# Optimization experiments

Hardware: AMD Instinct MI355X
Metric: run time of the kernel (lower is better)

The kernel has to match this reference:

```python
import jax, jax.numpy as jnp
import numpy as np

NEG_SLOPE = 0.2


def _seg_sum(x, ids, n):
    return jax.ops.segment_sum(x, ids, num_segments=n)


def _seg_softmax(score, ids, n):
    # numerically stable segment softmax over segments `ids`
    m = jax.ops.segment_max(score, ids, num_segments=n)
    ex = jnp.exp(score - m[ids])
    denom = _seg_sum(ex, ids, n)
    return ex / denom[ids]


def _seg_mean(x, ids, n):
    s = _seg_sum(x, ids, n)
    cnt = _seg_sum(jnp.ones(ids.shape[0], x.dtype), ids, n)
    return jnp.where(cnt[:, None] > 0, s / jnp.maximum(cnt, 1.0)[:, None], 0.0)


def _dphgnn(X, V, E, S, Wx, bx, Wv, bv, a, Wt, bt, num_nodes, num_edges):
    X_init = X @ Wx + bx                         # [N, H]
    X_feat = X @ Wv + bv                         # [N, H]
    score_node = X_feat @ a                      # [N]
    score = jax.nn.leaky_relu(score_node[V], NEG_SLOPE)   # [nnz]
    w = _seg_softmax(score, E, num_edges)        # [nnz]
    Xev = X_feat[V] * w[:, None]                 # [nnz, H] gather + weight
    Y_v2e = jax.nn.elu(_seg_sum(Xev, E, num_edges))       # [M, H]
    e_msg = jnp.concatenate([Y_v2e, S], axis=1)  # [M, H+star]
    Y = e_msg @ Wt + bt                          # [M, H]
    Xn = _seg_mean(Y[E], V, num_nodes)           # [N, H]
    Xn = jax.nn.elu(Xn)                          # is_last=False, dropout=eval
    return Xn + X_init


def _hyperconv(X, V, E, Wf, bf, num_nodes, num_edges):
    Xn = X @ Wf + bf
    Y = _seg_mean(Xn[V], E, num_edges)           # [M, O]
    ones = jnp.ones(V.shape[0], jnp.float32)
    D_v = _seg_sum(ones, V, num_nodes)           # node degrees
    cnt_e = _seg_sum(ones, E, num_edges)
    # torch scatter_reduce(mean, include_self=True): zero init counts as one element
    De = _seg_sum(D_v[V], E, num_edges) / (cnt_e + 1.0)
    De_inv = jnp.where(De > 0, De ** -0.5, 1.0)
    Y = De_inv[:, None] * Y
    Xo = _seg_sum(Y[E], V, num_nodes)
    Dv_inv = jnp.where(D_v > 0, D_v ** -0.5, 0.0)
    return Dv_inv[:, None] * Xo                  # is_last=True: no relu/dropout


def setup_inputs() -> dict:
    key = jax.random.key(0)
    ks = jax.random.split(key, 24)
    N, M, NNZ = 50000, 20000, 400000
    IN, H, OUT, STAR = 128, 256, 128, 64

    def lin(k, i, o):
        s = 1.0 / np.sqrt(i)
        k1, k2 = jax.random.split(k)
        return (jax.random.uniform(k1, (i, o), jnp.float32, -s, s),
                jax.random.uniform(k2, (o,), jnp.float32, -s, s))

    X = jax.random.normal(ks[0], (N, IN), jnp.float32)
    V = jax.random.randint(ks[1], (NNZ,), 0, N).at[-1].set(N - 1)
    E = jax.random.randint(ks[2], (NNZ,), 0, M).at[-1].set(M - 1)
    S = jax.random.normal(ks[3], (M, STAR), jnp.float32)

    Wx0, bx0 = lin(ks[4], IN, H)
    Wv0, bv0 = lin(ks[5], IN, H)
    a0 = jax.random.uniform(ks[6], (H,), jnp.float32, -1/np.sqrt(H), 1/np.sqrt(H))
    Wt0, bt0 = lin(ks[7], H + STAR, H)
    Wx1, bx1 = lin(ks[8], H, H)
    Wv1, bv1 = lin(ks[9], H, H)
    a1 = jax.random.uniform(ks[10], (H,), jnp.float32, -1/np.sqrt(H), 1/np.sqrt(H))
    Wt1, bt1 = lin(ks[11], H + STAR, H)
    Wf, bf = lin(ks[12], H, OUT)

    return dict(X=X, V=V, E=E, S=S,
                Wx0=Wx0, bx0=bx0, Wv0=Wv0, bv0=bv0, a0=a0, Wt0=Wt0, bt0=bt0,
                Wx1=Wx1, bx1=bx1, Wv1=Wv1, bv1=bv1, a1=a1, Wt1=Wt1, bt1=bt1,
                Wf=Wf, bf=bf)


def reference(X, V, E, S, Wx0, bx0, Wv0, bv0, a0, Wt0, bt0,
              Wx1, bx1, Wv1, bv1, a1, Wt1, bt1, Wf, bf):
    N = X.shape[0]
    M = S.shape[0]
    h = _dphgnn(X, V, E, S, Wx0, bx0, Wv0, bv0, a0, Wt0, bt0, N, M)
    h = _dphgnn(h, V, E, S, Wx1, bx1, Wv1, bv1, a1, Wt1, bt1, N, M)
    out = _hyperconv(h, V, E, Wf, bf, N, M)
    return out
```

## Files before the change

### kernel.cpp

```cpp
#include <hip/hip_runtime.h>

typedef unsigned short u16;
typedef __attribute__((ext_vector_type(4))) u16 u16x4;
typedef __attribute__((ext_vector_type(8))) u16 u16x8;
typedef __attribute__((ext_vector_type(8))) _Float16 f16x8;
typedef __attribute__((ext_vector_type(4))) float f32x4;

__device__ __forceinline__ u16 f2h(float x) {
    _Float16 h = (_Float16)x;
    return __builtin_bit_cast(u16, h);
}
__device__ __forceinline__ float h2f(u16 u) {
    return (float)__builtin_bit_cast(_Float16, u);
}

__device__ __forceinline__ void gl_lds16(const void* g, void* l) {
    __builtin_amdgcn_global_load_lds(
        (const __attribute__((address_space(1))) void*)g,
        (__attribute__((address_space(3))) void*)l, 16, 0, 0);
}

__global__ __launch_bounds__(256) void gemm_mfma_kernel(
    const u16* __restrict__ A, int lda,
    const u16* __restrict__ B, int ldb,
    const float* __restrict__ biasF, const float* __restrict__ biasB,
    u16* __restrict__ CbA, u16* __restrict__ CbB,
    const float* __restrict__ avec, float* __restrict__ scoreOut,
    const int* __restrict__ tKey, const int* __restrict__ tVal,
    int* __restrict__ tCur, int* __restrict__ tOut, int tNnz, int tailBlocks,
    int M, int Nc, int ncSplit, int K, int nrb, int ncb)
{
    if ((int)blockIdx.x < tailBlocks) {
        int k0 = ((int)blockIdx.x * 256 + (int)threadIdx.x) * 8;
        if (k0 >= tNnz) return;
        int kmax = min(tNnz - k0, 8);
        int kk[8], vv[8], sl[8];
        if (kmax == 8) {
            int4 a = *(const int4*)(tKey + k0), b = *(const int4*)(tKey + k0 + 4);
            int4 c = *(const int4*)(tVal + k0), d = *(const int4*)(tVal + k0 + 4);
            kk[0]=a.x; kk[1]=a.y; kk[2]=a.z; kk[3]=a.w; kk[4]=b.x; kk[5]=b.y; kk[6]=b.z; kk[7]=b.w;
            vv[0]=c.x; vv[1]=c.y; vv[2]=c.z; vv[3]=c.w; vv[4]=d.x; vv[5]=d.y; vv[6]=d.z; vv[7]=d.w;
        } else {
            for (int q = 0; q < kmax; ++q) { kk[q] = tKey[k0 + q]; vv[q] = tVal[k0 + q]; }
        }
        for (int q = 0; q < kmax; ++q) sl[q] = atomicAdd(&tCur[kk[q]], 1);
        for (int q = 0; q < kmax; ++q) tOut[sl[q]] = vv[q];
        return;
    }
    int g = (int)blockIdx.x - tailBlocks;
    int xcd = g & 7;
    int slot = g >> 3;
    int rbi = slot / ncb;
    int cb = slot - rbi * ncb;
    int rb = xcd + 8 * rbi;
    if (rb >= nrb) return;

    __shared__ __align__(16) u16 lds[12288];
    u16* sA0 = lds;
    u16* sA1 = lds + 4096;
    u16* sB0 = lds + 8192;
    u16* sB1 = lds + 10240;

    int tid = threadIdx.x;
    int wave = tid >> 6, lane = tid & 63;
    int row0 = rb * 128, col0 = cb * 64;

    long gA[2];
    int sOffA[2];
#pragma unroll
    for (int r = 0; r < 2; ++r) {
        int trow = r * 64 + wave * 16 + (lane >> 2);
        int chunk = (lane & 3) ^ ((trow >> 2) & 3);
        int arow = min(row0 + trow, M - 1);
        gA[r] = (long)arow * lda + chunk * 8;
        sOffA[r] = (r * 64 + wave * 16) * 32;
    }
    int trowB = wave * 16 + (lane >> 2);
    int chunkB = (lane & 3) ^ ((trowB >> 2) & 3);
    long gB = (long)(col0 + trowB) * ldb + chunkB * 8;
    int sOffB = (wave * 16) * 32;

    int m16 = lane & 15, quad = lane >> 4;
    int offA[4], offB[2];
#pragma unroll
    for (int i = 0; i < 4; ++i) {
        int ra = (wave & 1) * 64 + i * 16 + m16;
        offA[i] = ra * 32 + ((quad ^ ((ra >> 2) & 3)) * 8);
    }
#pragma unroll
    for (int j = 0; j < 2; ++j) {
        int rbx = (wave >> 1) * 32 + j * 16 + m16;
        offB[j] = rbx * 32 + ((quad ^ ((rbx >> 2) & 3)) * 8);
    }

    f32x4 acc[4][2];
#pragma unroll
    for (int i = 0; i < 4; ++i)
#pragma unroll
        for (int j = 0; j < 2; ++j) {
            f32x4 z = {0.f, 0.f, 0.f, 0.f};
            acc[i][j] = z;
        }

    int nkb = K >> 6;
    for (int kb = 0; kb < nkb; ++kb) {
#pragma unroll
        for (int r = 0; r < 2; ++r) {
            gl_lds16(A + gA[r], sA0 + sOffA[r]);
            gl_lds16(A + gA[r] + 32, sA1 + sOffA[r]);
        }
        gl_lds16(B + gB, sB0 + sOffB);
        gl_lds16(B + gB + 32, sB1 + sOffB);
        __syncthreads();
        {
            f16x8 av[4], bv[2];
#pragma unroll
            for (int i = 0; i < 4; ++i) av[i] = *(const f16x8*)(sA0 + offA[i]);
#pragma unroll
            for (int j = 0; j < 2; ++j) bv[j] = *(const f16x8*)(sB0 + offB[j]);
#pragma unroll
            for (int i = 0; i < 4; ++i)
#pragma unroll
                for (int j = 0; j < 2; ++j)
                    acc[i][j] = __builtin_amdgcn_mfma_f32_16x16x32_f16(av[i], bv[j], acc[i][j], 0, 0, 0);
        }
        {
            f16x8 av[4], bv[2];
#pragma unroll
            for (int i = 0; i < 4; ++i) av[i] = *(const f16x8*)(sA1 + offA[i]);
#pragma unroll
            for (int j = 0; j < 2; ++j) bv[j] = *(const f16x8*)(sB1 + offB[j]);
#pragma unroll
            for (int i = 0; i < 4; ++i)
#pragma unroll
                for (int j = 0; j < 2; ++j)
                    acc[i][j] = __builtin_amdgcn_mfma_f32_16x16x32_f16(av[i], bv[j], acc[i][j], 0, 0, 0);
        }
        __syncthreads();
#pragma unroll
        for (int r = 0; r < 2; ++r) gA[r] += 64;
        gB += 64;
    }

    int rbase = (wave & 1) * 64, cbase = (wave >> 1) * 32;
    float bj[2];
#pragma unroll
    for (int j = 0; j < 2; ++j) {
        int col = col0 + cbase + j * 16 + m16;
        bj[j] = (col >= ncSplit) ? biasB[col - ncSplit] : biasF[col];
    }
    u16* wlds = lds + wave * 2560;
    __syncthreads();
#pragma unroll
    for (int j = 0; j < 2; ++j)
#pragma unroll
        for (int i = 0; i < 4; ++i)
#pragma unroll
            for (int rr = 0; rr < 4; ++rr) {
                int lr = i * 16 + quad * 4 + rr;
                int lc = j * 16 + m16;
                int seg = (lc >> 3) ^ ((lr >> 2) & 3);
                wlds[lr * 40 + seg * 8 + (lc & 7)] = f2h(acc[i][j][rr] + bj[j]);
            }
    __syncthreads();
    {
        int colbase = col0 + cbase;
        bool isB = (colbase >= ncSplit);
        u16* Cp = isB ? CbB : CbA;
        int stride = isB ? (Nc - ncSplit) : ncSplit;
        int cc = isB ? (colbase - ncSplit) : colbase;
        bool doScore = (scoreOut != nullptr) && isB;
        int row = row0 + rbase + lane;
        if (row < M) {
            float sp = 0.f;
#pragma unroll
            for (int s = 0; s < 4; ++s) {
                int sseg = s ^ ((lane >> 2) & 3);
                u16x8 vv = *(const u16x8*)(wlds + lane * 40 + sseg * 8);
                *(u16x8*)(Cp + (size_t)row * stride + cc + s * 8) = vv;
                if (doScore) {
#pragma unroll
                    for (int q = 0; q < 8; ++q)
                        sp += h2f(vv[q]) * avec[cc + s * 8 + q];
                }
            }
            if (doScore) atomicAdd(scoreOut + row, sp);
        }
    }
}

struct WJob { const float* W; u16* Wt; int K; int ncShift; };
struct WJobs { WJob j[7]; };

__global__ void prep_fused_kernel(
    const int* __restrict__ V, const int* __restrict__ E,
    int* __restrict__ ecnt, int* __restrict__ ncnt, int nnz, int nbCnt,
    const float* __restrict__ X, u16* __restrict__ Abuf, int n4x,
    const float* __restrict__ S, u16* __restrict__ Ae, int nS, int nbCast,
    WJobs jobs)
{
    int b = blockIdx.x;
    if (b < nbCnt) {
        int k0 = (b * 256 + (int)threadIdx.x) * 8;
        if (k0 >= nnz) return;
        int kmax = min(nnz - k0, 8);
        int vv[8], ee[8];
        if (kmax == 8) {
            int4 a = *(const int4*)(V + k0), bb = *(const int4*)(V + k0 + 4);
            int4 c = *(const int4*)(E + k0), d = *(const int4*)(E + k0 + 4);
            vv[0]=a.x; vv[1]=a.y; vv[2]=a.z; vv[3]=a.w; vv[4]=bb.x; vv[5]=bb.y; vv[6]=bb.z; vv[7]=bb.w;
            ee[0]=c.x; ee[1]=c.y; ee[2]=c.z; ee[3]=c.w; ee[4]=d.x; ee[5]=d.y; ee[6]=d.z; ee[7]=d.w;
        } else {
            for (int q = 0; q < kmax; ++q) { vv[q] = V[k0 + q]; ee[q] = E[k0 + q]; }
        }
        for (int q = 0; q < kmax; ++q) atomicAdd(&ecnt[ee[q]], 1);
        for (int q = 0; q < kmax; ++q) atomicAdd(&ncnt[vv[q]], 1);
        return;
    }
    if (b < nbCnt + nbCast) {
        int id = (b - nbCnt) * 256 + (int)threadIdx.x;
        if (id < n4x) {
            float4 x = ((const float4*)X)[id];
            u16x4 h;
            h.x = f2h(x.x); h.y = f2h(x.y); h.z = f2h(x.z); h.w = f2h(x.w);
            *(u16x4*)(Abuf + (size_t)id * 4) = h;
        } else {
            int i = id - n4x;
            if (i < nS) {
                int e = i >> 6, c = i & 63;
                Ae[(size_t)e * 320 + 256 + c] = f2h(S[i]);
            }
        }
        return;
    }
    int bb = b - nbCnt - nbCast;
    int job = bb / 320, rem = bb - job * 320;
    WJob jb = jobs.j[job];
    int Nc = 1 << jb.ncShift;
    int idx = rem * 256 + (int)threadIdx.x;
    if (idx >= jb.K * Nc) return;
    int k = idx >> jb.ncShift, n = idx & (Nc - 1);
    jb.Wt[(size_t)n * jb.K + k] = f2h(jb.W[idx]);
}

__global__ __launch_bounds__(256) void scan_part1_dual(
    const int* __restrict__ cntE, int* __restrict__ offE, int* __restrict__ psumE, int nE, int nbE,
    const int* __restrict__ cntN, int* __restrict__ offN, int* __restrict__ psumN, int nN)
{
    const int* cnt; int* off; int* psum; int n; int b;
    if ((int)blockIdx.x < nbE) { cnt = cntE; off = offE; psum = psumE; n = nE; b = blockIdx.x; }
    else { cnt = cntN; off = offN; psum = psumN; n = nN; b = blockIdx.x - nbE; }

    __shared__ int tsum[256];
    int base = b * 1024;
    int t = threadIdx.x;
    int idx0 = base + t * 4;
    int4 c = make_int4(0, 0, 0, 0);
    if (idx0 + 3 < n) c = *(const int4*)(cnt + idx0);
    else {
        if (idx0 + 0 < n) c.x = cnt[idx0 + 0];
        if (idx0 + 1 < n) c.y = cnt[idx0 + 1];
        if (idx0 + 2 < n) c.z = cnt[idx0 + 2];
        if (idx0 + 3 < n) c.w = cnt[idx0 + 3];
    }
    int s = c.x + c.y + c.z + c.w;
    tsum[t] = s;
    __syncthreads();
    for (int o = 1; o < 256; o <<= 1) {
        int v = (t >= o) ? tsum[t - o] : 0;
        __syncthreads();
        tsum[t] += v;
        __syncthreads();
    }
    int run = tsum[t] - s;
    run += c.x; if (idx0 + 0 < n) off[idx0 + 1] = run;
    run += c.y; if (idx0 + 1 < n) off[idx0 + 2] = run;
    run += c.z; if (idx0 + 2 < n) off[idx0 + 3] = run;
    run += c.w; if (idx0 + 3 < n) off[idx0 + 4] = run;
    if (t == 255) psum[b] = tsum[255];
}

__global__ __launch_bounds__(256) void scan_part2_dual(
    const int* __restrict__ cntE, int* __restrict__ offE, const int* __restrict__ psumE,
    int* __restrict__ curE, int nE, int nbE,
    const int* __restrict__ cntN, int* __restrict__ offN, const int* __restrict__ psumN,
    int* __restrict__ curN, int nN)
{
    const int* cnt; int* off; const int* psum; int* cur; int n; int b;
    if ((int)blockIdx.x < nbE) { cnt = cntE; off = offE; psum = psumE; cur = curE; n = nE; b = blockIdx.x; }
    else { cnt = cntN; off = offN; psum = psumN; cur = curN; n = nN; b = blockIdx.x - nbE; }

    __shared__ int bpref;
    int t = threadIdx.x;
    if (t < 64) {
        int s = (t < b) ? psum[t] : 0;
#pragma unroll
        for (int o = 32; o; o >>= 1) s += __shfl_xor(s, o);
        if (t == 0) {
            bpref = s;
            if (b == 0) off[0] = 0;
        }
    }
    __syncthreads();
    int base = b * 1024 + t * 4;
#pragma unroll
    for (int q = 0; q < 4; ++q) {
        int i = base + q;
        if (i < n) {
            int inc = off[i + 1] + bpref;
            off[i + 1] = inc;
            cur[i] = inc - cnt[i];
        }
    }
}

__device__ __forceinline__ float lrelu(float s) { return s >= 0.f ? s : 0.2f * s; }

__global__ void v2e_fused_kernel(const u16* __restrict__ Xf,
                                 const float* __restrict__ score,
                                 const int* __restrict__ eoff,
                                 const int* __restrict__ edge_v,
                                 u16* __restrict__ Ae, int M)
{
    int e = blockIdx.x * 8 + (threadIdx.x >> 5);
    if (e >= M) return;
    int sl = threadIdx.x & 31;
    int j0 = eoff[e], j1 = eoff[e + 1];
    float m = -INFINITY;
    for (int j = j0 + sl; j < j1; j += 32) m = fmaxf(m, lrelu(score[edge_v[j]]));
#pragma unroll
    for (int o = 16; o; o >>= 1) m = fmaxf(m, __shfl_xor(m, o));
    float sum = 0.f;
    for (int j = j0 + sl; j < j1; j += 32) sum += expf(lrelu(score[edge_v[j]]) - m);
#pragma unroll
    for (int o = 16; o; o >>= 1) sum += __shfl_xor(sum, o);
    float inv = (j1 > j0) ? 1.0f / sum : 0.f;

    float acc[8] = {0.f, 0.f, 0.f, 0.f, 0.f, 0.f, 0.f, 0.f};
    int col = sl * 8;
    int j = j0;
    for (; j + 3 < j1; j += 4) {
        int v0 = edge_v[j + 0], v1 = edge_v[j + 1], v2 = edge_v[j + 2], v3 = edge_v[j + 3];
        float s0 = score[v0], s1 = score[v1], s2 = score[v2], s3 = score[v3];
        u16x8 r0 = *(const u16x8*)(Xf + (size_t)v0 * 256 + col);
        u16x8 r1 = *(const u16x8*)(Xf + (size_t)v1 * 256 + col);
        u16x8 r2 = *(const u16x8*)(Xf + (size_t)v2 * 256 + col);
        u16x8 r3 = *(const u16x8*)(Xf + (size_t)v3 * 256 + col);
        float w0 = expf(lrelu(s0) - m) * inv;
        float w1 = expf(lrelu(s1) - m) * inv;
        float w2 = expf(lrelu(s2) - m) * inv;
        float w3 = expf(lrelu(s3) - m) * inv;
#pragma unroll
        for (int q = 0; q < 8; ++q) {
            acc[q] += h2f(r0[q]) * w0;
            acc[q] += h2f(r1[q]) * w1;
            acc[q] += h2f(r2[q]) * w2;
            acc[q] += h2f(r3[q]) * w3;
        }
    }
    for (; j < j1; ++j) {
        int v = edge_v[j];
        float ww = expf(lrelu(score[v]) - m) * inv;
        u16x8 r = *(const u16x8*)(Xf + (size_t)v * 256 + col);
#pragma unroll
        for (int q = 0; q < 8; ++q) acc[q] += h2f(r[q]) * ww;
    }
    u16x8 hv;
#pragma unroll
    for (int q = 0; q < 8; ++q) {
        float vq = acc[q];
        vq = vq > 0.f ? vq : expm1f(vq);
        hv[q] = f2h(vq);
    }
    *(u16x8*)(Ae + (size_t)e * 320 + col) = hv;
}

__global__ void e2v_finish_kernel(const u16* __restrict__ Y,
                                  const int* __restrict__ noff,
                                  const int* __restrict__ node_e,
                                  const u16* __restrict__ Xinit,
                                  u16* __restrict__ H, int N,
                                  float* __restrict__ zbuf, int zN, int zTail)
{
    if ((int)blockIdx.x < zTail) {
        int id = (int)blockIdx.x * 256 + (int)threadIdx.x;
        if (id < zN) zbuf[id] = 0.f;
        return;
    }
    int v = ((int)blockIdx.x - zTail) * 8 + (threadIdx.x >> 5);
    if (v >= N) return;
    int sl = threadIdx.x & 31;
    int col = sl * 8;
    int i0 = noff[v], i1 = noff[v + 1];
    float acc[8] = {0.f, 0.f, 0.f, 0.f, 0.f, 0.f, 0.f, 0.f};
    int i = i0;
    for (; i + 3 < i1; i += 4) {
        int e0 = node_e[i + 0], e1 = node_e[i + 1], e2 = node_e[i + 2], e3 = node_e[i + 3];
        u16x8 r0 = *(const u16x8*)(Y + (size_t)e0 * 256 + col);
        u16x8 r1 = *(const u16x8*)(Y + (size_t)e1 * 256 + col);
        u16x8 r2 = *(const u16x8*)(Y + (size_t)e2 * 256 + col);
        u16x8 r3 = *(const u16x8*)(Y + (size_t)e3 * 256 + col);
#pragma unroll
        for (int q = 0; q < 8; ++q) {
            acc[q] += h2f(r0[q]);
            acc[q] += h2f(r1[q]);
            acc[q] += h2f(r2[q]);
            acc[q] += h2f(r3[q]);
        }
    }
    for (; i < i1; ++i) {
        int e = node_e[i];
        u16x8 r = *(const u16x8*)(Y + (size_t)e * 256 + col);
#pragma unroll
        for (int q = 0; q < 8; ++q) acc[q] += h2f(r[q]);
    }
    float inv = (i1 > i0) ? 1.0f / (float)(i1 - i0) : 0.f;
    size_t base = (size_t)v * 256 + col;
    u16x8 xi = *(const u16x8*)(Xinit + base);
    u16x8 hv;
#pragma unroll
    for (int q = 0; q < 8; ++q) {
        float mm = acc[q] * inv;
        float oq = (mm > 0.f ? mm : expm1f(mm)) + h2f(xi[q]);
        hv[q] = f2h(oq);
    }
    *(u16x8*)(H + base) = hv;
}

__global__ void yh_kernel(const u16* __restrict__ Xc,
                          const int* __restrict__ eoff, const int* __restrict__ edge_v,
                          const int* __restrict__ noff, u16* __restrict__ Yh, int M)
{
    int e = blockIdx.x * 16 + (threadIdx.x >> 4);
    if (e >= M) return;
    int sl = threadIdx.x & 15;
    int col = sl * 8;
    int j0 = eoff[e], j1 = eoff[e + 1];

    float dsum = 0.f;
    for (int j = j0 + sl; j < j1; j += 16) {
        int v = edge_v[j];
        dsum += (float)(noff[v + 1] - noff[v]);
    }
#pragma unroll
    for (int o = 8; o; o >>= 1) dsum += __shfl_xor(dsum, o);
    float De = dsum / ((float)(j1 - j0) + 1.0f);
    float deinv = De > 0.f ? rsqrtf(De) : 1.0f;

    float acc[8] = {0.f, 0.f, 0.f, 0.f, 0.f, 0.f, 0.f, 0.f};
    int j = j0;
    for (; j + 3 < j1; j += 4) {
        int v0 = edge_v[j + 0], v1 = edge_v[j + 1], v2 = edge_v[j + 2], v3 = edge_v[j + 3];
        u16x8 r0 = *(const u16x8*)(Xc + (size_t)v0 * 128 + col);
        u16x8 r1 = *(const u16x8*)(Xc + (size_t)v1 * 128 + col);
        u16x8 r2 = *(const u16x8*)(Xc + (size_t)v2 * 128 + col);
        u16x8 r3 = *(const u16x8*)(Xc + (size_t)v3 * 128 + col);
#pragma unroll
        for (int q = 0; q < 8; ++q) {
            acc[q] += h2f(r0[q]);
            acc[q] += h2f(r1[q]);
            acc[q] += h2f(r2[q]);
            acc[q] += h2f(r3[q]);
        }
    }
    for (; j < j1; ++j) {
        int v = edge_v[j];
        u16x8 r = *(const u16x8*)(Xc + (size_t)v * 128 + col);
#pragma unroll
        for (int q = 0; q < 8; ++q) acc[q] += h2f(r[q]);
    }
    float sc = ((j1 > j0) ? 1.0f / (float)(j1 - j0) : 0.f) * deinv;
    u16x8 o8;
#pragma unroll
    for (int q = 0; q < 8; ++q) o8[q] = f2h(acc[q] * sc);
    *(u16x8*)(Yh + (size_t)e * 128 + col) = o8;
}

__global__ void xo_final_kernel(const u16* __restrict__ Yh,
                                const int* __restrict__ noff, const int* __restrict__ node_e,
                                float* __restrict__ out, int N)
{
    int v = blockIdx.x * 16 + (threadIdx.x >> 4);
    if (v >= N) return;
    int sl = threadIdx.x & 15;
    int col = sl * 8;
    int i0 = noff[v], i1 = noff[v + 1];
    float acc[8] = {0.f, 0.f, 0.f, 0.f, 0.f, 0.f, 0.f, 0.f};
    int i = i0;
    for (; i + 3 < i1; i += 4) {
        int e0 = node_e[i + 0], e1 = node_e[i + 1], e2 = node_e[i + 2], e3 = node_e[i + 3];
        u16x8 r0 = *(const u16x8*)(Yh + (size_t)e0 * 128 + col);
        u16x8 r1 = *(const u16x8*)(Yh + (size_t)e1 * 128 + col);
        u16x8 r2 = *(const u16x8*)(Yh + (size_t)e2 * 128 + col);
        u16x8 r3 = *(const u16x8*)(Yh + (size_t)e3 * 128 + col);
#pragma unroll
        for (int q = 0; q < 8; ++q) {
            acc[q] += h2f(r0[q]);
            acc[q] += h2f(r1[q]);
            acc[q] += h2f(r2[q]);
            acc[q] += h2f(r3[q]);
        }
    }
    for (; i < i1; ++i) {
        int e = node_e[i];
        u16x8 r = *(const u16x8*)(Yh + (size_t)e * 128 + col);
#pragma unroll
        for (int q = 0; q < 8; ++q) acc[q] += h2f(r[q]);
    }
    float sc = (i1 > i0) ? rsqrtf((float)(i1 - i0)) : 0.f;
    float4 oA, oB;
    oA.x = acc[0] * sc; oA.y = acc[1] * sc; oA.z = acc[2] * sc; oA.w = acc[3] * sc;
    oB.x = acc[4] * sc; oB.y = acc[5] * sc; oB.z = acc[6] * sc; oB.w = acc[7] * sc;
    float* d = out + (size_t)v * 128 + col;
    *(float4*)d = oA;
    *(float4*)(d + 4) = oB;
}

static void gemm(const u16* A, int lda,
                 const u16* B, int ldb,
                 const float* biasF, const float* biasB,
                 u16* CbA, u16* CbB,
                 const float* avec, float* scoreOut,
                 const int* tKey, const int* tVal, int* tCur, int* tOut, int tNnz,
                 int M, int Nc, int ncSplit, int K,
                 hipStream_t stream)
{
    int nrb = (M + 127) / 128, ncb = Nc / 64;
    int nrb8 = ((nrb + 7) / 8) * 8;
    int tailBlocks = (tKey != nullptr) ? (tNnz + 2047) / 2048 : 0;
    gemm_mfma_kernel<<<nrb8 * ncb + tailBlocks, 256, 0, stream>>>(
        A, lda, B, ldb, biasF, biasB, CbA, CbB, avec, scoreOut,
        tKey, tVal, tCur, tOut, tNnz, tailBlocks, M, Nc, ncSplit, K, nrb, ncb);
}

extern "C" void kernel_launch(void* const* d_in, const int* in_sizes, int n_in,
                              void* d_out, int out_size, void* d_ws, size_t ws_size,
                              hipStream_t stream)
{
    const float* X   = (const float*)d_in[0];
    const int*   V   = (const int*)d_in[1];
    const int*   E   = (const int*)d_in[2];
    const float* S   = (const float*)d_in[3];
    const float* Wx0 = (const float*)d_in[4];  const float* bx0 = (const float*)d_in[5];
    const float* Wv0 = (const float*)d_in[6];  const float* bv0 = (const float*)d_in[7];
    const float* a0  = (const float*)d_in[8];
    const float* Wt0 = (const float*)d_in[9];  const float* bt0 = (const float*)d_in[10];
    const float* Wx1 = (const float*)d_in[11]; const float* bx1 = (const float*)d_in[12];
    const float* Wv1 = (const float*)d_in[13]; const float* bv1 = (const float*)d_in[14];
    const float* a1  = (const float*)d_in[15];
    const float* Wt1 = (const float*)d_in[16]; const float* bt1 = (const float*)d_in[17];
    const float* Wf  = (const float*)d_in[18]; const float* bf  = (const float*)d_in[19];

    int N   = in_sizes[0] / 128;
    int NNZ = in_sizes[1];
    int M   = in_sizes[3] / 64;

    float* ws = (float*)d_ws;
    size_t off = 0;
    u16* XinitB = (u16*)(ws + off); off += (size_t)N * 128;
    u16* XfeatR = (u16*)(ws + off); off += (size_t)N * 128;
    u16* Xfeatb = XfeatR;
    u16* Ybufb  = XfeatR;
    u16* Abuf = (u16*)(ws + off); off += (size_t)N * 128;
    u16* Ae   = (u16*)(ws + off); off += (size_t)M * 160;
    u16* WxvT0 = (u16*)(ws + off); off += (size_t)(512 * 128) / 2;
    u16* WtT0  = (u16*)(ws + off); off += (size_t)(256 * 320) / 2;
    u16* WxvT1 = (u16*)(ws + off); off += (size_t)(512 * 256) / 2;
    u16* WtT1  = (u16*)(ws + off); off += (size_t)(256 * 320) / 2;
    u16* WfT   = (u16*)(ws + off); off += (size_t)(128 * 256) / 2;
    int* ecnt   = (int*)(ws + off); off += (size_t)M;
    int* ncnt   = (int*)(ws + off); off += (size_t)N;
    float* score = ws + off;        off += (size_t)N;
    int* eoff   = (int*)(ws + off); off += (size_t)(M + 1);
    int* ecur   = (int*)(ws + off); off += (size_t)M;
    int* psumE  = (int*)(ws + off); off += 64;
    int* edge_v = (int*)(ws + off); off += (size_t)NNZ;
    int* noff   = (int*)(ws + off); off += (size_t)(N + 1);
    int* ncur   = (int*)(ws + off); off += (size_t)N;
    int* psumN  = (int*)(ws + off); off += 64;
    int* node_e = (int*)(ws + off); off += (size_t)NNZ;

    hipMemsetAsync(ecnt, 0, (size_t)(M + 2 * N) * 4, stream);

    int n4x = N * 128 / 4, nS = M * 64;
    int nbCnt = (NNZ + 2047) / 2048;
    int nbCast = (n4x + nS + 255) / 256;
    WJobs jobs;
    jobs.j[0] = {Wx0, WxvT0,             128, 8};
    jobs.j[1] = {Wv0, WxvT0 + 256 * 128, 128, 8};
    jobs.j[2] = {Wt0, WtT0,              320, 8};
    jobs.j[3] = {Wx1, WxvT1,             256, 8};
    jobs.j[4] = {Wv1, WxvT1 + 256 * 256, 256, 8};
    jobs.j[5] = {Wt1, WtT1,              320, 8};
    jobs.j[6] = {Wf,  WfT,               256, 7};
    int nbW = 7 * 320;
    prep_fused_kernel<<<nbCnt + nbCast + nbW, 256, 0, stream>>>(
        V, E, ecnt, ncnt, NNZ, nbCnt, X, Abuf, n4x, S, Ae, nS, nbCast, jobs);

    int nbE = (M + 1023) / 1024, nbN = (N + 1023) / 1024;
    scan_part1_dual<<<nbE + nbN, 256, 0, stream>>>(ecnt, eoff, psumE, M, nbE,
                                                   ncnt, noff, psumN, N);
    scan_part2_dual<<<nbE + nbN, 256, 0, stream>>>(ecnt, eoff, psumE, ecur, M, nbE,
                                                   ncnt, noff, psumN, ncur, N);

    gemm(Abuf, 128, WxvT0, 128, bx0, bv0, XinitB, Xfeatb, a0, score,
         E, V, ecur, edge_v, NNZ, N, 512, 256, 128, stream);
    v2e_fused_kernel<<<(M + 7) / 8, 256, 0, stream>>>(Xfeatb, score, eoff, edge_v, Ae, M);
    gemm(Ae, 320, WtT0, 320, nullptr, bt0, nullptr, Ybufb, nullptr, nullptr,
         V, E, ncur, node_e, NNZ, M, 256, 0, 320, stream);
    {
        int zTail = (N + 255) / 256;
        e2v_finish_kernel<<<zTail + (N + 7) / 8, 256, 0, stream>>>(
            Ybufb, noff, node_e, XinitB, Abuf, N, score, N, zTail);
    }

    gemm(Abuf, 256, WxvT1, 256, bx1, bv1, XinitB, Xfeatb, a1, score,
         nullptr, nullptr, nullptr, nullptr, 0, N, 512, 256, 256, stream);
    v2e_fused_kernel<<<(M + 7) / 8, 256, 0, stream>>>(Xfeatb, score, eoff, edge_v, Ae, M);
    gemm(Ae, 320, WtT1, 320, nullptr, bt1, nullptr, Ybufb, nullptr, nullptr,
         nullptr, nullptr, nullptr, nullptr, 0, M, 256, 0, 320, stream);
    e2v_finish_kernel<<<(N + 7) / 8, 256, 0, stream>>>(
        Ybufb, noff, node_e, XinitB, Abuf, N, nullptr, 0, 0);

    u16* Xcb = XfeatR;
    u16* Yhb = XinitB;
    gemm(Abuf, 256, WfT, 256, bf, nullptr, Xcb, nullptr, nullptr, nullptr,
         nullptr, nullptr, nullptr, nullptr, 0, N, 128, 128, 256, stream);
    yh_kernel<<<(M + 15) / 16, 256, 0, stream>>>(Xcb, eoff, edge_v, noff, Yhb, M);
    xo_final_kernel<<<(N + 15) / 16, 256, 0, stream>>>(Yhb, noff, node_e, (float*)d_out, N);
}
```

Before: 467.6 us.

## Build CSR via atomic ranks in counting pass, fill without second atomic pass

The degree-counting atomics move from the prep kernel into the tail blocks of the first GEMM, and each atomic's return value is kept as the entry's rank within its segment. After the scan, a new non-atomic fill kernel writes edge_v and node_e at offset plus rank. This replaces the later atomic scatter passes that were spread across two GEMM launches, and scan_part2 no longer writes cursor arrays. The cost is two extra NNZ-sized rank arrays, one extra kernel launch, and a different placement of the counting work in the schedule.

Result: faster. 438.0 us (-6.3%).

```diff
diff --git a/kernel.cpp b/kernel.cpp
--- a/kernel.cpp
+++ b/kernel.cpp
@@ -26,25 +26,39 @@
     const float* __restrict__ biasF, const float* __restrict__ biasB,
     u16* __restrict__ CbA, u16* __restrict__ CbB,
     const float* __restrict__ avec, float* __restrict__ scoreOut,
-    const int* __restrict__ tKey, const int* __restrict__ tVal,
-    int* __restrict__ tCur, int* __restrict__ tOut, int tNnz, int tailBlocks,
+    const int* __restrict__ cV, const int* __restrict__ cE,
+    int* __restrict__ ecnt, int* __restrict__ ncnt,
+    int* __restrict__ rankE, int* __restrict__ rankN, int tNnz, int tailBlocks,
     int M, int Nc, int ncSplit, int K, int nrb, int ncb)
 {
     if ((int)blockIdx.x < tailBlocks) {
         int k0 = ((int)blockIdx.x * 256 + (int)threadIdx.x) * 8;
         if (k0 >= tNnz) return;
         int kmax = min(tNnz - k0, 8);
-        int kk[8], vv[8], sl[8];
+        int vv[8], ee[8], rE[8], rN[8];
         if (kmax == 8) {
-            int4 a = *(const int4*)(tKey + k0), b = *(const int4*)(tKey + k0 + 4);
-            int4 c = *(const int4*)(tVal + k0), d = *(const int4*)(tVal + k0 + 4);
-            kk[0]=a.x; kk[1]=a.y; kk[2]=a.z; kk[3]=a.w; kk[4]=b.x; kk[5]=b.y; kk[6]=b.z; kk[7]=b.w;
-            vv[0]=c.x; vv[1]=c.y; vv[2]=c.z; vv[3]=c.w; vv[4]=d.x; vv[5]=d.y; vv[6]=d.z; vv[7]=d.w;
+            int4 a = *(const int4*)(cV + k0), b = *(const int4*)(cV + k0 + 4);
+            int4 c = *(const int4*)(cE + k0), d = *(const int4*)(cE + k0 + 4);
+            vv[0]=a.x; vv[1]=a.y; vv[2]=a.z; vv[3]=a.w; vv[4]=b.x; vv[5]=b.y; vv[6]=b.z; vv[7]=b.w;
+            ee[0]=c.x; ee[1]=c.y; ee[2]=c.z; ee[3]=c.w; ee[4]=d.x; ee[5]=d.y; ee[6]=d.z; ee[7]=d.w;
         } else {
-            for (int q = 0; q < kmax; ++q) { kk[q] = tKey[k0 + q]; vv[q] = tVal[k0 + q]; }
-        }
-        for (int q = 0; q < kmax; ++q) sl[q] = atomicAdd(&tCur[kk[q]], 1);
-        for (int q = 0; q < kmax; ++q) tOut[sl[q]] = vv[q];
+            for (int q = 0; q < kmax; ++q) { vv[q] = cV[k0 + q]; ee[q] = cE[k0 + q]; }
+        }
+        for (int q = 0; q < kmax; ++q) rE[q] = atomicAdd(&ecnt[ee[q]], 1);
+        for (int q = 0; q < kmax; ++q) rN[q] = atomicAdd(&ncnt[vv[q]], 1);
+        if (kmax == 8) {
+            int4 r0, r1;
+            r0.x=rE[0]; r0.y=rE[1]; r0.z=rE[2]; r0.w=rE[3];
+            r1.x=rE[4]; r1.y=rE[5]; r1.z=rE[6]; r1.w=rE[7];
+            *(int4*)(rankE + k0) = r0;
+            *(int4*)(rankE + k0 + 4) = r1;
+            r0.x=rN[0]; r0.y=rN[1]; r0.z=rN[2]; r0.w=rN[3];
+            r1.x=rN[4]; r1.y=rN[5]; r1.z=rN[6]; r1.w=rN[7];
+            *(int4*)(rankN + k0) = r0;
+            *(int4*)(rankN + k0 + 4) = r1;
+        } else {
+            for (int q = 0; q < kmax; ++q) { rankE[k0 + q] = rE[q]; rankN[k0 + q] = rN[q]; }
+        }
         return;
     }
     int g = (int)blockIdx.x - tailBlocks;
@@ -193,32 +207,13 @@
 struct WJobs { WJob j[7]; };
 
 __global__ void prep_fused_kernel(
-    const int* __restrict__ V, const int* __restrict__ E,
-    int* __restrict__ ecnt, int* __restrict__ ncnt, int nnz, int nbCnt,
     const float* __restrict__ X, u16* __restrict__ Abuf, int n4x,
     const float* __restrict__ S, u16* __restrict__ Ae, int nS, int nbCast,
     WJobs jobs)
 {
     int b = blockIdx.x;
-    if (b < nbCnt) {
-        int k0 = (b * 256 + (int)threadIdx.x) * 8;
-        if (k0 >= nnz) return;
-        int kmax = min(nnz - k0, 8);
-        int vv[8], ee[8];
-        if (kmax == 8) {
-            int4 a = *(const int4*)(V + k0), bb = *(const int4*)(V + k0 + 4);
-            int4 c = *(const int4*)(E + k0), d = *(const int4*)(E + k0 + 4);
-            vv[0]=a.x; vv[1]=a.y; vv[2]=a.z; vv[3]=a.w; vv[4]=bb.x; vv[5]=bb.y; vv[6]=bb.z; vv[7]=bb.w;
-            ee[0]=c.x; ee[1]=c.y; ee[2]=c.z; ee[3]=c.w; ee[4]=d.x; ee[5]=d.y; ee[6]=d.z; ee[7]=d.w;
-        } else {
-            for (int q = 0; q < kmax; ++q) { vv[q] = V[k0 + q]; ee[q] = E[k0 + q]; }
-        }
-        for (int q = 0; q < kmax; ++q) atomicAdd(&ecnt[ee[q]], 1);
-        for (int q = 0; q < kmax; ++q) atomicAdd(&ncnt[vv[q]], 1);
-        return;
-    }
-    if (b < nbCnt + nbCast) {
-        int id = (b - nbCnt) * 256 + (int)threadIdx.x;
+    if (b < nbCast) {
+        int id = b * 256 + (int)threadIdx.x;
         if (id < n4x) {
             float4 x = ((const float4*)X)[id];
             u16x4 h;
@@ -233,7 +228,7 @@
         }
         return;
     }
-    int bb = b - nbCnt - nbCast;
+    int bb = b - nbCast;
     int job = bb / 320, rem = bb - job * 320;
     WJob jb = jobs.j[job];
     int Nc = 1 << jb.ncShift;
@@ -281,14 +276,12 @@
 }
 
 __global__ __launch_bounds__(256) void scan_part2_dual(
-    const int* __restrict__ cntE, int* __restrict__ offE, const int* __restrict__ psumE,
-    int* __restrict__ curE, int nE, int nbE,
-    const int* __restrict__ cntN, int* __restrict__ offN, const int* __restrict__ psumN,
-    int* __restrict__ curN, int nN)
-{
-    const int* cnt; int* off; const int* psum; int* cur; int n; int b;
-    if ((int)blockIdx.x < nbE) { cnt = cntE; off = offE; psum = psumE; cur = curE; n = nE; b = blockIdx.x; }
-    else { cnt = cntN; off = offN; psum = psumN; cur = curN; n = nN; b = blockIdx.x - nbE; }
+    int* __restrict__ offE, const int* __restrict__ psumE, int nE, int nbE,
+    int* __restrict__ offN, const int* __restrict__ psumN, int nN)
+{
+    int* off; const int* psum; int n; int b;
+    if ((int)blockIdx.x < nbE) { off = offE; psum = psumE; n = nE; b = blockIdx.x; }
+    else { off = offN; psum = psumN; n = nN; b = blockIdx.x - nbE; }
 
     __shared__ int bpref;
     int t = threadIdx.x;
@@ -306,10 +299,36 @@
 #pragma unroll
     for (int q = 0; q < 4; ++q) {
         int i = base + q;
-        if (i < n) {
-            int inc = off[i + 1] + bpref;
-            off[i + 1] = inc;
-            cur[i] = inc - cnt[i];
+        if (i < n) off[i + 1] += bpref;
+    }
+}
+
+__global__ void fill_ranked_kernel(const int* __restrict__ V, const int* __restrict__ E,
+                                   const int* __restrict__ rankE, const int* __restrict__ rankN,
+                                   const int* __restrict__ eoff, const int* __restrict__ noff,
+                                   int* __restrict__ edge_v, int* __restrict__ node_e, int nnz)
+{
+    int k0 = (blockIdx.x * blockDim.x + threadIdx.x) * 4;
+    if (k0 >= nnz) return;
+    int kmax = min(nnz - k0, 4);
+    if (kmax == 4) {
+        int4 v4 = *(const int4*)(V + k0);
+        int4 e4 = *(const int4*)(E + k0);
+        int4 re = *(const int4*)(rankE + k0);
+        int4 rn = *(const int4*)(rankN + k0);
+        edge_v[eoff[e4.x] + re.x] = v4.x;
+        edge_v[eoff[e4.y] + re.y] = v4.y;
+        edge_v[eoff[e4.z] + re.z] = v4.z;
+        edge_v[eoff[e4.w] + re.w] = v4.w;
+        node_e[noff[v4.x] + rn.x] = e4.x;
+        node_e[noff[v4.y] + rn.y] = e4.y;
+        node_e[noff[v4.z] + rn.z] = e4.z;
+        node_e[noff[v4.w] + rn.w] = e4.w;
+    } else {
+        for (int q = 0; q < kmax; ++q) {
+            int v = V[k0 + q], e = E[k0 + q];
+            edge_v[eoff[e] + rankE[k0 + q]] = v;
+            node_e[noff[v] + rankN[k0 + q]] = e;
         }
     }
 }
@@ -521,16 +540,17 @@
                  const float* biasF, const float* biasB,
                  u16* CbA, u16* CbB,
                  const float* avec, float* scoreOut,
-                 const int* tKey, const int* tVal, int* tCur, int* tOut, int tNnz,
+                 const int* cV, const int* cE, int* ecnt, int* ncnt,
+                 int* rankE, int* rankN, int tNnz,
                  int M, int Nc, int ncSplit, int K,
                  hipStream_t stream)
 {
     int nrb = (M + 127) / 128, ncb = Nc / 64;
     int nrb8 = ((nrb + 7) / 8) * 8;
-    int tailBlocks = (tKey != nullptr) ? (tNnz + 2047) / 2048 : 0;
+    int tailBlocks = (cV != nullptr) ? (tNnz + 2047) / 2048 : 0;
     gemm_mfma_kernel<<<nrb8 * ncb + tailBlocks, 256, 0, stream>>>(
         A, lda, B, ldb, biasF, biasB, CbA, CbB, avec, scoreOut,
-        tKey, tVal, tCur, tOut, tNnz, tailBlocks, M, Nc, ncSplit, K, nrb, ncb);
+        cV, cE, ecnt, ncnt, rankE, rankN, tNnz, tailBlocks, M, Nc, ncSplit, K, nrb, ncb);
 }
 
 extern "C" void kernel_launch(void* const* d_in, const int* in_sizes, int n_in,
@@ -572,18 +592,17 @@
     int* ncnt   = (int*)(ws + off); off += (size_t)N;
     float* score = ws + off;        off += (size_t)N;
     int* eoff   = (int*)(ws + off); off += (size_t)(M + 1);
-    int* ecur   = (int*)(ws + off); off += (size_t)M;
     int* psumE  = (int*)(ws + off); off += 64;
     int* edge_v = (int*)(ws + off); off += (size_t)NNZ;
     int* noff   = (int*)(ws + off); off += (size_t)(N + 1);
-    int* ncur   = (int*)(ws + off); off += (size_t)N;
     int* psumN  = (int*)(ws + off); off += 64;
     int* node_e = (int*)(ws + off); off += (size_t)NNZ;
+    int* rankE  = (int*)(ws + off); off += (size_t)NNZ;
+    int* rankN  = (int*)(ws + off); off += (size_t)NNZ;
 
     hipMemsetAsync(ecnt, 0, (size_t)(M + 2 * N) * 4, stream);
 
     int n4x = N * 128 / 4, nS = M * 64;
-    int nbCnt = (NNZ + 2047) / 2048;
     int nbCast = (n4x + nS + 255) / 256;
     WJobs jobs;
     jobs.j[0] = {Wx0, WxvT0,             128, 8};
@@ -594,20 +613,24 @@
     jobs.j[5] = {Wt1, WtT1,              320, 8};
     jobs.j[6] = {Wf,  WfT,               256, 7};
     int nbW = 7 * 320;
-    prep_fused_kernel<<<nbCnt + nbCast + nbW, 256, 0, stream>>>(
-        V, E, ecnt, ncnt, NNZ, nbCnt, X, Abuf, n4x, S, Ae, nS, nbCast, jobs);
+    prep_fused_kernel<<<nbCast + nbW, 256, 0, stream>>>(
+        X, Abuf, n4x, S, Ae, nS, nbCast, jobs);
+
+    gemm(Abuf, 128, WxvT0, 128, bx0, bv0, XinitB, Xfeatb, a0, score,
+         V, E, ecnt, ncnt, rankE, rankN, NNZ, N, 512, 256, 128, stream);
 
     int nbE = (M + 1023) / 1024, nbN = (N + 1023) / 1024;
     scan_part1_dual<<<nbE + nbN, 256, 0, stream>>>(ecnt, eoff, psumE, M, nbE,
                                                    ncnt, noff, psumN, N);
-    scan_part2_dual<<<nbE + nbN, 256, 0, stream>>>(ecnt, eoff, psumE, ecur, M, nbE,
-                                                   ncnt, noff, psumN, ncur, N);
-
-    gemm(Abuf, 128, WxvT0, 128, bx0, bv0, XinitB, Xfeatb, a0, score,
-         E, V, ecur, edge_v, NNZ, N, 512, 256, 128, stream);
+    scan_part2_dual<<<nbE + nbN, 256, 0, stream>>>(eoff, psumE, M, nbE,
+                                                   noff, psumN, N);
+
+    fill_ranked_kernel<<<((NNZ + 3) / 4 + 255) / 256, 256, 0, stream>>>(
+        V, E, rankE, rankN, eoff, noff, edge_v, node_e, NNZ);
+
     v2e_fused_kernel<<<(M + 7) / 8, 256, 0, stream>>>(Xfeatb, score, eoff, edge_v, Ae, M);
     gemm(Ae, 320, WtT0, 320, nullptr, bt0, nullptr, Ybufb, nullptr, nullptr,
-         V, E, ncur, node_e, NNZ, M, 256, 0, 320, stream);
+         nullptr, nullptr, nullptr, nullptr, nullptr, nullptr, 0, M, 256, 0, 320, stream);
     {
         int zTail = (N + 255) / 256;
         e2v_finish_kernel<<<zTail + (N + 7) / 8, 256, 0, stream>>>(
@@ -615,17 +638,17 @@
     }
 
     gemm(Abuf, 256, WxvT1, 256, bx1, bv1, XinitB, Xfeatb, a1, score,
-         nullptr, nullptr, nullptr, nullptr, 0, N, 512, 256, 256, stream);
+         nullptr, nullptr, nullptr, nullptr, nullptr, nullptr, 0, N, 512, 256, 256, stream);
     v2e_fused_kernel<<<(M + 7) / 8, 256, 0, stream>>>(Xfeatb, score, eoff, edge_v, Ae, M);
     gemm(Ae, 320, WtT1, 320, nullptr, bt1, nullptr, Ybufb, nullptr, nullptr,
-         nullptr, nullptr, nullptr, nullptr, 0, M, 256, 0, 320, stream);
+         nullptr, nullptr, nullptr, nullptr, nullptr, nullptr, 0, M, 256, 0, 320, stream);
     e2v_finish_kernel<<<(N + 7) / 8, 256, 0, stream>>>(
         Ybufb, noff, node_e, XinitB, Abuf, N, nullptr, 0, 0);
 
     u16* Xcb = XfeatR;
     u16* Yhb = XinitB;
     gemm(Abuf, 256, WfT, 256, bf, nullptr, Xcb, nullptr, nullptr, nullptr,
-         nullptr, nullptr, nullptr, nullptr, 0, N, 128, 128, 256, stream);
+         nullptr, nullptr, nullptr, nullptr, nullptr, nullptr, 0, N, 128, 128, 256, stream);
     yh_kernel<<<(M + 15) / 16, 256, 0, stream>>>(Xcb, eoff, edge_v, noff, Yhb, M);
     xo_final_kernel<<<(N + 15) / 16, 256, 0, stream>>>(Yhb, noff, node_e, (float*)d_out, N);
 }
```
